# Kernel tuning notes

Measured on AMD Instinct MI355X. Metric: run time of the kernel, lower is better.

## Reference

```python
import jax, jax.numpy as jnp
import numpy as np

RATIO = 2          # BigVGAN Activation1d up/down ratio
K_FILT = 12        # int(6 * ratio // 2) * 2
DILATIONS = (1, 3, 5)


def _kaiser_sinc_filter1d(cutoff, half_width, kernel_size):
    # Faithful port of BigVGAN's kaiser_sinc_filter1d (even kernel path).
    half_size = kernel_size // 2
    delta_f = 4.0 * half_width
    A = 2.285 * (half_size - 1) * np.pi * delta_f + 7.95
    if A > 50.0:
        beta = 0.1102 * (A - 8.7)
    elif A >= 21.0:
        beta = 0.5842 * (A - 21.0) ** 0.4 + 0.07886 * (A - 21.0)
    else:
        beta = 0.0
    window = np.kaiser(kernel_size, beta)              # periodic=False
    time = np.arange(-half_size, half_size) + 0.5       # even kernel size
    filt = 2.0 * cutoff * window * np.sinc(2.0 * cutoff * time)
    filt = filt / filt.sum()
    return jnp.asarray(filt, dtype=jnp.float32)

FILT = _kaiser_sinc_filter1d(0.5 / RATIO, 0.6 / RATIO, K_FILT)


def _depthwise1d(x, filt, stride, lhs_dilation, padding):
    # x: (B, T, C), filt: (k,) shared across channels (depthwise)
    C = x.shape[-1]
    kern = jnp.tile(filt[:, None, None], (1, 1, C))  # (k, 1, C)
    return jax.lax.conv_general_dilated(
        x, kern, window_strides=(stride,), padding=padding,
        lhs_dilation=(lhs_dilation,), feature_group_count=C,
        dimension_numbers=('NLC', 'LIO', 'NLC'))


def upsample2(x):
    # BigVGAN UpSample1d(ratio=2): replicate pad -> conv_transpose -> crop
    pad = K_FILT // RATIO - 1                       # 5
    pad_left = pad * RATIO + (K_FILT - RATIO) // 2  # 15
    pad_right = pad * RATIO + (K_FILT - RATIO + 1) // 2  # 15
    x = jnp.pad(x, ((0, 0), (pad, pad), (0, 0)), mode='edge')
    # conv_transpose(stride=r) == lhs-dilated conv with full padding
    # (filter is symmetric, so no flip needed)
    y = RATIO * _depthwise1d(x, FILT, 1, RATIO, [(K_FILT - 1, K_FILT - 1)])
    return y[:, pad_left:-pad_right, :]  # (B, 2T, C)


def downsample2(x):
    # BigVGAN DownSample1d(ratio=2) == LowPassFilter1d(stride=2)
    pad_left = K_FILT // 2 - 1  # 5 (even kernel)
    pad_right = K_FILT // 2     # 6
    x = jnp.pad(x, ((0, 0), (pad_left, pad_right), (0, 0)), mode='edge')
    return _depthwise1d(x, FILT, RATIO, 1, 'VALID')  # (B, T, C)


def snake(x, log_alpha):
    # alpha_logscale=True: alpha = exp(param); x + (1/alpha) sin^2(alpha x)
    alpha = jnp.exp(log_alpha)  # (C,), broadcasts over (B, T, C)
    return x + (1.0 / (alpha + 1e-9)) * jnp.square(jnp.sin(alpha * x))


def act1d(x, log_alpha):
    return downsample2(snake(upsample2(x), log_alpha))


def wn_conv(x, v, g, b, dilation):
    # weight-norm: kernel = v / ||v||_(0,1) * g, then SAME dilated conv
    norm = jnp.linalg.norm(v, axis=(0, 1))[None, None, :]  # (1,1,Cout)
    kern = (v / norm) * g  # (k, Cin, Cout)
    y = jax.lax.conv_general_dilated(
        x, kern, window_strides=(1,), padding='SAME',
        rhs_dilation=(dilation,), dimension_numbers=('NLC', 'LIO', 'NLC'))
    return y + b


def setup_inputs() -> dict:
    key = jax.random.key(0)
    ks = jax.random.split(key, 7)
    B, T, C, K = 4, 8192, 512, 3
    n = len(DILATIONS)
    x = jax.random.normal(ks[0], (B, T, C), dtype=jnp.float32)
    v1 = jax.random.normal(ks[1], (n, K, C, C), dtype=jnp.float32)
    g1 = jax.random.uniform(ks[2], (n, 1, 1, C), dtype=jnp.float32)
    b1 = 0.01 * jax.random.normal(ks[3], (n, C), dtype=jnp.float32)
    v2 = jax.random.normal(ks[4], (n, K, C, C), dtype=jnp.float32)
    g2 = jax.random.uniform(ks[5], (n, 1, 1, C), dtype=jnp.float32)
    b2 = 0.01 * jax.random.normal(ks[6], (n, C), dtype=jnp.float32)
    alphas = jnp.zeros((2 * n, C), dtype=jnp.float32)  # log-alpha init 0
    return {'x': x, 'v1': v1, 'g1': g1, 'b1': b1,
            'v2': v2, 'g2': g2, 'b2': b2, 'alphas': alphas}


def reference(x, v1, g1, b1, v2, g2, b2, alphas):
    for i, d in enumerate(DILATIONS):
        xt = act1d(x, alphas[2 * i])
        xt = wn_conv(xt, v1[i], g1[i], b1[i], d)
        xt = act1d(xt, alphas[2 * i + 1])
        xt = wn_conv(xt, v2[i], g2[i], b2[i], 1)
        x = xt + x
    return x
```

## Files before the change

### kernel.cpp

```cpp
#include <hip/hip_runtime.h>
#include <math.h>

#define TLEN   8192
#define CCH    512
#define NBATCH 4
#define GUARD_B 8
#define GUARD_T 16
#define XROWS  (TLEN + GUARD_B + GUARD_T)

typedef __attribute__((ext_vector_type(8))) short short8;
typedef __attribute__((ext_vector_type(4))) float f32x4;

struct Filt { float f[12]; };

#define MFMA16(a, b, c) __builtin_amdgcn_mfma_f32_16x16x32_bf16(a, b, c, 0, 0, 0)

__device__ __forceinline__ unsigned short f2bf(float f) {
  unsigned u = __float_as_uint(f);
  unsigned r = (u + 0x7fffu + ((u >> 16) & 1u)) >> 16;
  return (unsigned short)r;
}

__device__ __forceinline__ float bf2f(unsigned short u) {
  return __uint_as_float((unsigned)u << 16);
}

__device__ __forceinline__ float fast_sin(float x) {
  float r = x * 0.15915494309189535f;
  r -= floorf(r);
  return __builtin_amdgcn_sinf(r);
}

__device__ __forceinline__ float snake1(float u, float a, float rcp) {
  float s = fast_sin(a * u);
  return fmaf(rcp * s, s, u);
}

__device__ __forceinline__ void gload16(const void* g, void* l) {
  __builtin_amdgcn_global_load_lds(
      (const __attribute__((address_space(1))) unsigned int*)g,
      (__attribute__((address_space(3))) unsigned int*)l, 16, 0, 0);
}

__global__ __launch_bounds__(256)
void normp_k(const float* __restrict__ v1, const float* __restrict__ v2,
             float* __restrict__ part) {
  __shared__ float red[256];
  const int c  = blockIdx.x;
  const int cc = blockIdx.y;
  const int jc = blockIdx.z;
  const int col = threadIdx.x & 63;
  const int js  = threadIdx.x >> 6;
  const int co = cc * 64 + col;
  const float* v = (c < 3) ? v1 + (size_t)c * 3 * CCH * CCH
                           : v2 + (size_t)(c - 3) * 3 * CCH * CCH;
  const int j0 = jc * 64 + js * 16;
  float s = 0.f;
  #pragma unroll
  for (int jj = 0; jj < 16; ++jj) {
    float w = v[(size_t)(j0 + jj) * CCH + co];
    s = fmaf(w, w, s);
  }
  red[threadIdx.x] = s;
  __syncthreads();
  if (threadIdx.x < 64) {
    float t = red[threadIdx.x] + red[threadIdx.x + 64] +
              red[threadIdx.x + 128] + red[threadIdx.x + 192];
    part[(size_t)(c * CCH + co) * 24 + jc] = t;
  }
}

__global__ __launch_bounds__(256)
void fin_k(const float* __restrict__ part, const float* __restrict__ g1,
           const float* __restrict__ g2, float* __restrict__ scl) {
  const int i = blockIdx.x * 256 + threadIdx.x;
  const int c = i >> 9, co = i & 511;
  float s = 0.f;
  #pragma unroll
  for (int jc = 0; jc < 24; ++jc) s += part[(size_t)i * 24 + jc];
  const float g = (c < 3) ? g1[c * CCH + co] : g2[(c - 3) * CCH + co];
  scl[i] = g / sqrtf(s);
}

__global__ __launch_bounds__(512)
void zguard_k(unsigned short* __restrict__ xb) {
  const int b = blockIdx.x / 24;
  const int g = blockIdx.x % 24;
  const int row = (g < 8) ? g : (TLEN + g);
  xb[((size_t)b * XROWS + row) * CCH + threadIdx.x] = 0;
}

__global__ __launch_bounds__(256)
void wprep_k(const float* __restrict__ v1, const float* __restrict__ v2,
             const float* __restrict__ scl, unsigned short* __restrict__ wp) {
  const int gtid = blockIdx.x * 256 + threadIdx.x;
  const int lane = gtid & 63;
  const int gw = gtid >> 6;
  const int c  = gw / 1536;
  int r = gw - c * 1536;
  const int tap = r >> 9;  r &= 511;
  const int cib = r >> 6;  r &= 63;
  const int cob = r >> 4;
  const int cb  = r & 15;
  const int nf = cb >> 1, kk = cb & 1;
  const int co  = cob * 128 + nf * 16 + (lane & 15);
  const int ci0 = cib * 64 + kk * 32 + (lane >> 4) * 8;
  const float* v = (c < 3) ? v1 + (size_t)c * 3 * CCH * CCH
                           : v2 + (size_t)(c - 3) * 3 * CCH * CCH;
  const float s = scl[c * CCH + co];
  unsigned short o[8];
  #pragma unroll
  for (int j = 0; j < 8; ++j) {
    float w = v[((size_t)tap * CCH + ci0 + j) * CCH + co] * s;
    o[j] = f2bf(w);
  }
  *reinterpret_cast<short8*>(wp + (size_t)gw * 512 + lane * 8) =
      *reinterpret_cast<const short8*>(o);
}

template<int INBF>
__global__ __launch_bounds__(256)
void act_k(const void* __restrict__ xin, unsigned short* __restrict__ y,
           const float* __restrict__ la, Filt F) {
  const int idx = blockIdx.x * 256 + threadIdx.x;
  const int c  = (idx & 127) << 2;
  const int ts = (idx >> 7) & 2047;
  const int b  = idx >> 18;
  const int t0 = ts * 4;

  auto ldrow = [&](int row) -> f32x4 {
    if constexpr (INBF) {
      const unsigned short* p =
          (const unsigned short*)xin + ((size_t)b * TLEN + row) * CCH + c;
      ushort4 u = *reinterpret_cast<const ushort4*>(p);
      f32x4 r;
      r[0] = bf2f(u.x); r[1] = bf2f(u.y); r[2] = bf2f(u.z); r[3] = bf2f(u.w);
      return r;
    } else {
      const float* p = (const float*)xin + ((size_t)b * TLEN + row) * CCH + c;
      return *reinterpret_cast<const f32x4*>(p);
    }
  };

  float av[4], rv[4];
  #pragma unroll
  for (int ch = 0; ch < 4; ++ch) {
    av[ch] = expf(la[c + ch]);
    rv[ch] = 1.f / (av[ch] + 1e-9f);
  }

  float acc[4][4];

  if (ts >= 2 && ts <= 2045) {
    f32x4 xw[14];
    #pragma unroll
    for (int j = 0; j < 14; ++j) xw[j] = ldrow(t0 - 5 + j);

    #pragma unroll
    for (int ch = 0; ch < 4; ++ch) {
      float s[18];
      #pragma unroll
      for (int mi = 0; mi < 18; ++mi) {
        float u = 0.f;
        if (mi & 1) {
          const int base = (mi - 5) / 2 + 2;
          #pragma unroll
          for (int r = 0; r < 6; ++r) u = fmaf(F.f[2*r], xw[base + r][ch], u);
        } else {
          const int base = (mi - 6) / 2 + 3;
          #pragma unroll
          for (int r = 0; r < 6; ++r) u = fmaf(F.f[2*r+1], xw[base + r][ch], u);
        }
        u *= 2.f;
        s[mi] = snake1(u, av[ch], rv[ch]);
      }
      #pragma unroll
      for (int tt = 0; tt < 4; ++tt) {
        float a = 0.f;
        #pragma unroll
        for (int k = 0; k < 12; ++k) a = fmaf(F.f[k], s[2*tt + k], a);
        acc[tt][ch] = a;
      }
    }
  } else {
    #pragma unroll
    for (int tt = 0; tt < 4; ++tt) {
      const int t = t0 + tt;
      float a0=0.f, a1=0.f, a2=0.f, a3=0.f;
      for (int k = 0; k < 12; ++k) {
        int m  = 2*t + k - 5;
        int mc = m < 0 ? 0 : (m > 2*TLEN - 1 ? 2*TLEN - 1 : m);
        int tp = mc >> 1;
        int odd = mc & 1;
        float u0=0.f,u1=0.f,u2=0.f,u3=0.f;
        #pragma unroll
        for (int r = 0; r < 6; ++r) {
          int i  = odd ? (tp + r - 2) : (tp + r - 3);
          int ic = i < 0 ? 0 : (i > TLEN - 1 ? TLEN - 1 : i);
          float tap = odd ? F.f[2*r+1] : F.f[2*r];
          f32x4 xv = ldrow(ic);
          u0 = fmaf(tap, xv[0], u0); u1 = fmaf(tap, xv[1], u1);
          u2 = fmaf(tap, xv[2], u2); u3 = fmaf(tap, xv[3], u3);
        }
        u0 *= 2.f; u1 *= 2.f; u2 *= 2.f; u3 *= 2.f;
        const float fk = F.f[k];
        a0 = fmaf(fk, snake1(u0,av[0],rv[0]), a0);
        a1 = fmaf(fk, snake1(u1,av[1],rv[1]), a1);
        a2 = fmaf(fk, snake1(u2,av[2],rv[2]), a2);
        a3 = fmaf(fk, snake1(u3,av[3],rv[3]), a3);
      }
      acc[tt][0]=a0; acc[tt][1]=a1; acc[tt][2]=a2; acc[tt][3]=a3;
    }
  }

  #pragma unroll
  for (int tt = 0; tt < 4; ++tt) {
    ushort4 o;
    o.x = f2bf(acc[tt][0]); o.y = f2bf(acc[tt][1]);
    o.z = f2bf(acc[tt][2]); o.w = f2bf(acc[tt][3]);
    *reinterpret_cast<ushort4*>(
        y + ((size_t)b * XROWS + GUARD_B + t0 + tt) * CCH + c) = o;
  }
}

template<int DIL, int OB>
__global__ __launch_bounds__(256)
void convm_k(const unsigned short* __restrict__ xb,
             const unsigned short* __restrict__ wp,
             const float* __restrict__ bia,
             const float* __restrict__ res,
             float* __restrict__ outf,
             unsigned short* __restrict__ outb) {
  __shared__ unsigned short As[2][144 * 64];
  __shared__ unsigned short Bs[2][16 * 512];

  const int tid  = threadIdx.x;
  const int lane = tid & 63;
  const int wid  = tid >> 6;
  const int wr = wid >> 1, wc = wid & 1;

  const int l   = (blockIdx.x & 7) * 128 + (blockIdx.x >> 3);
  const int coB = l & 3;
  const int tb  = l >> 2;
  const int b   = tb >> 6;
  const int t0  = (tb & 63) * 128;
  const int co0 = coB * 128;

  const int qq = lane >> 4;
  const int r0 = lane & 15;

  const int a_r = lane >> 3;
  const int a_c = (lane & 7) ^ a_r;
  const unsigned short* xrow0 =
      xb + ((size_t)b * XROWS + GUARD_B + t0 - DIL) * CCH;

  f32x4 acc[4][4] = {};

  auto stageA = [&](int cib, int buf) {
    #pragma unroll
    for (int u = 0; u < 5; ++u) {
      const int i = wid + u * 4;
      if (i < 18) {
        const unsigned short* g =
            xrow0 + (size_t)(8 * i + a_r) * CCH + cib * 64 + a_c * 8;
        gload16(g, &As[buf][i * 512]);
      }
    }
  };
  auto stageB = [&](int tap, int cib, int buf) {
    #pragma unroll
    for (int u = 0; u < 4; ++u) {
      const int cb = wid * 4 + u;
      const unsigned short* g =
          wp + ((((size_t)(tap * 8 + cib) * 4 + coB) * 16 + cb) * 512) + lane * 8;
      gload16(g, &Bs[buf][cb * 512]);
    }
  };
  auto compute = [&](int tap, int pa, int pb) {
    const int rowbase = tap * DIL + wr * 64 + r0;
    const int xr = (tap * DIL + r0) & 7;
    #pragma unroll
    for (int kk = 0; kk < 2; ++kk) {
      const int coff = 8 * ((kk * 4 + qq) ^ xr);
      short8 af[4], bf[4];
      #pragma unroll
      for (int i = 0; i < 4; ++i)
        af[i] = *reinterpret_cast<const short8*>(
            &As[pa][(rowbase + i * 16) * 64 + coff]);
      #pragma unroll
      for (int j = 0; j < 4; ++j)
        bf[j] = *reinterpret_cast<const short8*>(
            &Bs[pb][((wc * 4 + j) * 2 + kk) * 512 + lane * 8]);
      #pragma unroll
      for (int i = 0; i < 4; ++i)
        #pragma unroll
        for (int j = 0; j < 4; ++j)
          acc[i][j] = MFMA16(af[i], bf[j], acc[i][j]);
    }
  };

  stageA(0, 0);
  stageB(0, 0, 0);
  __syncthreads();

  int pa = 0, pb = 0;
  for (int cib = 0; cib < 8; ++cib) {
    #pragma unroll
    for (int tap = 0; tap < 3; ++tap) {
      if (tap < 2) {
        stageB(tap + 1, cib, pb ^ 1);
      } else if (cib < 7) {
        stageB(0, cib + 1, pb ^ 1);
        stageA(cib + 1, pa ^ 1);
      }
      compute(tap, pa, pb);
      __syncthreads();
      pb ^= 1;
    }
    pa ^= 1;
  }

  #pragma unroll
  for (int j = 0; j < 4; ++j) {
    const int co = co0 + (wc * 4 + j) * 16 + r0;
    const float bv = bia[co];
    #pragma unroll
    for (int i = 0; i < 4; ++i) {
      const int t = t0 + (wr * 4 + i) * 16 + qq * 4;
      #pragma unroll
      for (int e = 0; e < 4; ++e) {
        const size_t off = ((size_t)b * TLEN + t + e) * CCH + co;
        float o = acc[i][j][e] + bv;
        if constexpr (OB) {
          outb[off] = f2bf(o);
        } else {
          if (res) o += res[off];
          outf[off] = o;
        }
      }
    }
  }
}

static double bessel_i0(double x) {
  double t = 1.0, s = 1.0, q = x * x * 0.25;
  for (int k = 1; k < 64; ++k) {
    t *= q / ((double)k * (double)k);
    s += t;
    if (t < 1e-18 * s) break;
  }
  return s;
}

static void make_filter(Filt* F) {
  const double cutoff = 0.25, hw = 0.3;
  const int ks = 12, half = 6;
  const double A = 2.285 * (half - 1) * M_PI * (4.0 * hw) + 7.95;
  double beta;
  if (A > 50.0)       beta = 0.1102 * (A - 8.7);
  else if (A >= 21.0) beta = 0.5842 * pow(A - 21.0, 0.4) + 0.07886 * (A - 21.0);
  else                beta = 0.0;
  const double i0b = bessel_i0(beta);
  double f[12], sum = 0.0;
  for (int n = 0; n < 12; ++n) {
    double rr = 2.0 * n / (ks - 1) - 1.0;
    double w  = bessel_i0(beta * sqrt(fmax(0.0, 1.0 - rr * rr))) / i0b;
    double tm = (double)(n - half) + 0.5;
    double sx = 2.0 * cutoff * tm;
    double snc = (sx == 0.0) ? 1.0 : sin(M_PI * sx) / (M_PI * sx);
    f[n] = 2.0 * cutoff * w * snc;
    sum += f[n];
  }
  for (int n = 0; n < 12; ++n) F->f[n] = (float)(f[n] / sum);
}

extern "C" void kernel_launch(void* const* d_in, const int* in_sizes, int n_in,
                              void* d_out, int out_size, void* d_ws, size_t ws_size,
                              hipStream_t stream) {
  (void)in_sizes; (void)n_in; (void)out_size; (void)ws_size;
  const float* x  = (const float*)d_in[0];
  const float* v1 = (const float*)d_in[1];
  const float* g1 = (const float*)d_in[2];
  const float* b1 = (const float*)d_in[3];
  const float* v2 = (const float*)d_in[4];
  const float* g2 = (const float*)d_in[5];
  const float* b2 = (const float*)d_in[6];
  const float* al = (const float*)d_in[7];
  float* out = (float*)d_out;

  const size_t N = (size_t)NBATCH * TLEN * CCH;
  unsigned short* wb1  = (unsigned short*)d_ws;
  unsigned short* xbuf = wb1 + N;
  unsigned short* wp   = xbuf + (size_t)NBATCH * XROWS * CCH;
  float* part = (float*)(wp + (size_t)6 * 3 * CCH * CCH);
  float* scl  = part + (size_t)6 * CCH * 24;

  Filt F;
  make_filter(&F);

  zguard_k<<<96, 512, 0, stream>>>(xbuf);
  normp_k<<<dim3(6, 8, 24), 256, 0, stream>>>(v1, v2, part);
  fin_k<<<12, 256, 0, stream>>>(part, g1, g2, scl);
  wprep_k<<<2304, 256, 0, stream>>>(v1, v2, scl, wp);

  const int cgrid = NBATCH * (TLEN / 128) * 4;
  const int nblk_act = (NBATCH * 2048 * 128) / 256;
  const size_t wsz = (size_t)3 * CCH * CCH;

  for (int i = 0; i < 3; ++i) {
    const float* xsrc = (i == 0) ? x : out;
    act_k<0><<<nblk_act, 256, 0, stream>>>(xsrc, xbuf, al + (size_t)(2 * i) * CCH, F);
    if (i == 0)
      convm_k<1, 1><<<cgrid, 256, 0, stream>>>(xbuf, wp + 0 * wsz, b1 + 0 * CCH,
                                               nullptr, nullptr, wb1);
    else if (i == 1)
      convm_k<3, 1><<<cgrid, 256, 0, stream>>>(xbuf, wp + 1 * wsz, b1 + 1 * CCH,
                                               nullptr, nullptr, wb1);
    else
      convm_k<5, 1><<<cgrid, 256, 0, stream>>>(xbuf, wp + 2 * wsz, b1 + 2 * CCH,
                                               nullptr, nullptr, wb1);
    act_k<1><<<nblk_act, 256, 0, stream>>>(wb1, xbuf, al + (size_t)(2 * i + 1) * CCH, F);
    convm_k<1, 0><<<cgrid, 256, 0, stream>>>(xbuf, wp + (3 + i) * wsz, b2 + i * CCH,
                                             xsrc, out, nullptr);
  }
}
```

Measured before the change: 702.4 us.

## Load conv weight fragments directly from global into registers, drop B LDS staging

```diff
diff --git a/kernel.cpp b/kernel.cpp
--- a/kernel.cpp
+++ b/kernel.cpp
@@ -224,7 +224,7 @@
 }
 
 template<int DIL, int OB>
-__global__ __launch_bounds__(256)
+__global__ __launch_bounds__(256, 3)
 void convm_k(const unsigned short* __restrict__ xb,
              const unsigned short* __restrict__ wp,
              const float* __restrict__ bia,
@@ -232,7 +232,6 @@
              float* __restrict__ outf,
              unsigned short* __restrict__ outb) {
   __shared__ unsigned short As[2][144 * 64];
-  __shared__ unsigned short Bs[2][16 * 512];
 
   const int tid  = threadIdx.x;
   const int lane = tid & 63;
@@ -253,6 +252,9 @@
   const int a_c = (lane & 7) ^ a_r;
   const unsigned short* xrow0 =
       xb + ((size_t)b * XROWS + GUARD_B + t0 - DIL) * CCH;
+
+  const unsigned short* wpB =
+      wp + ((size_t)coB * 16 + wc * 8) * 512 + lane * 8;
 
   f32x4 acc[4][4] = {};
 
@@ -267,56 +269,44 @@
       }
     }
   };
-  auto stageB = [&](int tap, int cib, int buf) {
-    #pragma unroll
-    for (int u = 0; u < 4; ++u) {
-      const int cb = wid * 4 + u;
-      const unsigned short* g =
-          wp + ((((size_t)(tap * 8 + cib) * 4 + coB) * 16 + cb) * 512) + lane * 8;
-      gload16(g, &Bs[buf][cb * 512]);
-    }
-  };
-  auto compute = [&](int tap, int pa, int pb) {
+
+  auto dotap = [&](int tap, int cib, int buf) {
+    const unsigned short* gB = wpB + ((size_t)(tap * 8 + cib) * 64) * 512;
+    short8 bf[8];
+    #pragma unroll
+    for (int j = 0; j < 4; ++j)
+      #pragma unroll
+      for (int kk = 0; kk < 2; ++kk)
+        bf[j * 2 + kk] = *reinterpret_cast<const short8*>(
+            gB + (size_t)(j * 2 + kk) * 512);
     const int rowbase = tap * DIL + wr * 64 + r0;
     const int xr = (tap * DIL + r0) & 7;
     #pragma unroll
     for (int kk = 0; kk < 2; ++kk) {
       const int coff = 8 * ((kk * 4 + qq) ^ xr);
-      short8 af[4], bf[4];
+      short8 af[4];
       #pragma unroll
       for (int i = 0; i < 4; ++i)
         af[i] = *reinterpret_cast<const short8*>(
-            &As[pa][(rowbase + i * 16) * 64 + coff]);
-      #pragma unroll
-      for (int j = 0; j < 4; ++j)
-        bf[j] = *reinterpret_cast<const short8*>(
-            &Bs[pb][((wc * 4 + j) * 2 + kk) * 512 + lane * 8]);
+            &As[buf][(rowbase + i * 16) * 64 + coff]);
       #pragma unroll
       for (int i = 0; i < 4; ++i)
         #pragma unroll
         for (int j = 0; j < 4; ++j)
-          acc[i][j] = MFMA16(af[i], bf[j], acc[i][j]);
+          acc[i][j] = MFMA16(af[i], bf[j * 2 + kk], acc[i][j]);
     }
   };
 
   stageA(0, 0);
-  stageB(0, 0, 0);
   __syncthreads();
 
-  int pa = 0, pb = 0;
+  int pa = 0;
   for (int cib = 0; cib < 8; ++cib) {
-    #pragma unroll
-    for (int tap = 0; tap < 3; ++tap) {
-      if (tap < 2) {
-        stageB(tap + 1, cib, pb ^ 1);
-      } else if (cib < 7) {
-        stageB(0, cib + 1, pb ^ 1);
-        stageA(cib + 1, pa ^ 1);
-      }
-      compute(tap, pa, pb);
-      __syncthreads();
-      pb ^= 1;
-    }
+    if (cib < 7) stageA(cib + 1, pa ^ 1);
+    dotap(0, cib, pa);
+    dotap(1, cib, pa);
+    dotap(2, cib, pa);
+    __syncthreads();
     pa ^= 1;
   }
 
@@ -326,7 +316,7 @@
     const float bv = bia[co];
     #pragma unroll
     for (int i = 0; i < 4; ++i) {
-      const int t = t0 + (wr * 4 + i) * 16 + qq * 4;
+      const int t = t0 + wr * 64 + i * 16 + qq * 4;
       #pragma unroll
       for (int e = 0; e < 4; ++e) {
         const size_t off = ((size_t)b * TLEN + t + e) * CCH + co;
```

Measured after the change: 713.5 us. About the same (+1.6%).
